# Kernel optimization log

Measured on AMD Instinct MI355X. Metric: run time of the kernel, lower is better.

## Reference

```python
import jax, jax.numpy as jnp
import numpy as np

B = 2048
MAX_ATOMS = 32
ELEM = 83
LATENT = 64
LATTICE = 9


def _lin(k, fin, fout):
    k1, k2 = jax.random.split(k)
    s = 1.0 / np.sqrt(fin)
    return (jax.random.uniform(k1, (fin, fout), jnp.float32, -s, s),
            jax.random.uniform(k2, (fout,), jnp.float32, -s, s))


def setup_inputs() -> dict:
    key = jax.random.key(0)
    ks = jax.random.split(key, 32)
    inp = {}
    inp['elements'] = jax.random.randint(ks[0], (B, MAX_ATOMS), 0, ELEM)
    inp['coords'] = jax.random.uniform(ks[1], (B, MAX_ATOMS, 3), jnp.float32)
    inp['lattice'] = jax.random.normal(ks[2], (B, LATTICE), jnp.float32)
    inp['composition'] = jax.random.uniform(ks[3], (B, ELEM), jnp.float32)
    inp['eps'] = jax.random.normal(ks[4], (B, LATENT), jnp.float32)
    inp['emb_table'] = jax.random.normal(ks[5], (ELEM, 16), jnp.float32)
    inp['enc_w1'], inp['enc_b1'] = _lin(ks[6], 19, 256)
    inp['enc_w2'], inp['enc_b2'] = _lin(ks[7], 256, 128)
    inp['enc_w3'], inp['enc_b3'] = _lin(ks[8], 128, 128)
    inp['lat_w1'], inp['lat_b1'] = _lin(ks[9], LATTICE, 64)
    inp['lat_w2'], inp['lat_b2'] = _lin(ks[10], 64, 64)
    inp['mu_w'], inp['mu_b'] = _lin(ks[11], 192, LATENT)
    inp['lv_w'], inp['lv_b'] = _lin(ks[12], 192, LATENT)
    inp['dec_w1'], inp['dec_b1'] = _lin(ks[13], LATENT + ELEM, 512)
    s1 = 1.0 / np.sqrt(64 * 27)
    inp['ct1_w'] = jax.random.uniform(ks[14], (32, 64, 3, 3, 3), jnp.float32, -s1, s1)
    inp['ct1_b'] = jax.random.uniform(ks[15], (32,), jnp.float32, -s1, s1)
    s2 = 1.0 / np.sqrt(32 * 27)
    inp['ct2_w'] = jax.random.uniform(ks[16], (16, 32, 3, 3, 3), jnp.float32, -s2, s2)
    inp['ct2_b'] = jax.random.uniform(ks[17], (16,), jnp.float32, -s2, s2)
    inp['dec_w2'], inp['dec_b2'] = _lin(ks[18], 16 * 8 * 8 * 8, MAX_ATOMS * (ELEM + 3))
    inp['dl_w1'], inp['dl_b1'] = _lin(ks[19], LATENT, 64)
    inp['dl_w2'], inp['dl_b2'] = _lin(ks[20], 64, LATTICE)
    inp['gat1_w'], _ = _lin(ks[21], 19, 3 * 64)
    inp['gat1_b'] = jnp.zeros((3 * 64,), jnp.float32)
    inp['gat1_as'] = jax.random.normal(ks[22], (3, 64), jnp.float32) * 0.1
    inp['gat1_ad'] = jax.random.normal(ks[23], (3, 64), jnp.float32) * 0.1
    inp['gat2_w'], _ = _lin(ks[24], 192, 3)
    inp['gat2_b'] = jnp.zeros((3,), jnp.float32)
    inp['gat2_as'] = jax.random.normal(ks[25], (1, 3), jnp.float32) * 0.1
    inp['gat2_ad'] = jax.random.normal(ks[26], (1, 3), jnp.float32) * 0.1
    return inp


def _convT(x, w, b):
    # ConvTranspose3d(k=3, stride=2, pad=1, output_pad=1) == input-dilated conv
    y = jax.lax.conv_general_dilated(
        x, w, window_strides=(1, 1, 1),
        padding=((1, 2), (1, 2), (1, 2)), lhs_dilation=(2, 2, 2),
        dimension_numbers=('NCDHW', 'OIDHW', 'NCDHW'))
    return y + b[None, :, None, None, None]


def _gat(x, W, a_src, a_dst, bias, heads, out_ch, concat):
    # Dense (fully-connected per-sample graph) GATConv, eval mode (dropout off).
    Bn, N, F = x.shape
    h = jnp.einsum('bnf,fhc->bnhc', x, W.reshape(F, heads, out_ch))  # [B,N,H,C]
    s = jnp.einsum('bnhc,hc->bnh', h, a_src)  # source scores
    d = jnp.einsum('bnhc,hc->bnh', h, a_dst)  # target scores
    # e[b,i,j,h] for edge j->i (self-loops included in the full mesh)
    e = jax.nn.leaky_relu(d[:, :, None, :] + s[:, None, :, :], 0.2)
    a = jax.nn.softmax(e, axis=2)  # softmax over sources j per target i
    o = jnp.einsum('bijh,bjhc->bihc', a, h)
    if concat:
        return o.reshape(Bn, N, heads * out_ch) + bias
    return o.mean(axis=2) + bias


def reference(elements, coords, lattice, composition, eps, emb_table,
              enc_w1, enc_b1, enc_w2, enc_b2, enc_w3, enc_b3,
              lat_w1, lat_b1, lat_w2, lat_b2, mu_w, mu_b, lv_w, lv_b,
              dec_w1, dec_b1, ct1_w, ct1_b, ct2_w, ct2_b, dec_w2, dec_b2,
              dl_w1, dl_b1, dl_w2, dl_b2,
              gat1_w, gat1_b, gat1_as, gat1_ad,
              gat2_w, gat2_b, gat2_as, gat2_ad):
    Bn = coords.shape[0]
    # ---- encode ----
    af = jnp.concatenate([emb_table[elements], coords], axis=-1)  # [B,32,19]
    h = jax.nn.relu(af @ enc_w1 + enc_b1)
    h = jax.nn.relu(h @ enc_w2 + enc_b2)
    h = h @ enc_w3 + enc_b3
    g = h.mean(axis=1)  # [B,128]
    l = jax.nn.relu(lattice @ lat_w1 + lat_b1) @ lat_w2 + lat_b2
    comb = jnp.concatenate([g, l], axis=1)
    mu = comb @ mu_w + mu_b
    logvar = comb @ lv_w + lv_b
    z = mu + eps * jnp.exp(0.5 * logvar)
    # ---- decode ----
    d = jnp.concatenate([z, composition], axis=1) @ dec_w1 + dec_b1
    d = d.reshape(Bn, 64, 2, 2, 2)
    d = jax.nn.relu(_convT(d, ct1_w, ct1_b))   # [B,32,4,4,4]
    d = jax.nn.relu(_convT(d, ct2_w, ct2_b))   # [B,16,8,8,8]
    raw = (d.reshape(Bn, -1) @ dec_w2 + dec_b2).reshape(Bn, MAX_ATOMS, ELEM + 3)
    logits = raw[..., :ELEM]
    init_coords = jax.nn.sigmoid(raw[..., ELEM:])
    node = jnp.concatenate([emb_table[jnp.argmax(logits, axis=-1)], init_coords], axis=-1)  # [B,32,19]
    x = jax.nn.elu(_gat(node, gat1_w, gat1_as, gat1_ad, gat1_b, 3, 64, True))
    adj = jnp.tanh(_gat(x, gat2_w, gat2_as, gat2_ad, gat2_b, 1, 3, False)) * 0.1
    coords_out = jnp.mod(init_coords + adj, 1.0)
    recon = jnp.concatenate([logits, coords_out], axis=-1)  # [B,32,86]
    recon_lattice = jax.nn.relu(z @ dl_w1 + dl_b1) @ dl_w2 + dl_b2
    return (mu, logvar, recon, recon_lattice)
```

## Files before the change

### kernel.cpp

```cpp
#include <hip/hip_runtime.h>
#include <hip/hip_bf16.h>

typedef __hip_bfloat16 bf16;
typedef __attribute__((ext_vector_type(8))) __bf16 bf16x8;
typedef __attribute__((ext_vector_type(4))) float f32x4;

__device__ __forceinline__ float b2f(bf16 v){ return __bfloat162float(v); }
__device__ __forceinline__ bf16  f2b(float v){ return __float2bfloat16(v); }

template<typename T> __device__ __forceinline__ float ldf(const T* p, size_t i);
template<> __device__ __forceinline__ float ldf<float>(const float* p, size_t i){ return p[i]; }
template<> __device__ __forceinline__ float ldf<bf16 >(const bf16*  p, size_t i){ return b2f(p[i]); }

template<typename T> __device__ __forceinline__ void stf(T* p, size_t i, float v);
template<> __device__ __forceinline__ void stf<float>(float* p, size_t i, float v){ p[i] = v; }
template<> __device__ __forceinline__ void stf<bf16 >(bf16*  p, size_t i, float v){ p[i] = f2b(v); }

#define NATM 32
#define RECON_OFF 262144
#define RL_OFF    5898240

__device__ __forceinline__ void glds16(const bf16* g, bf16* l){
    __builtin_amdgcn_global_load_lds(
        (const __attribute__((address_space(1))) unsigned int*)g,
        (__attribute__((address_space(3))) unsigned int*)l,
        16, 0, 0);
}

__global__ __launch_bounds__(64) void k_detect(const void* emb, int* flag)
{
    __shared__ int cnt[64];
    const int t = threadIdx.x;
    const unsigned short* p = (const unsigned short*)emb;
    int c = 0;
    for (int i = t; i < 256; i += 64){
        int e = (p[i] >> 7) & 0xFF;
        c += (e >= 110 && e <= 132) ? 1 : 0;
    }
    cnt[t] = c;
    __syncthreads();
    if (t == 0){
        int s = 0;
        for (int i = 0; i < 64; i++) s += cnt[i];
        *flag = (s >= 200) ? 1 : 0;
    }
}

template<typename T>
__device__ __forceinline__ void enc_impl(
    const int* elements, const T* coords, const T* emb,
    const T* w1, const T* b1, const T* w2, const T* b2c,
    const T* w3, const T* b3, float* gbuf, char* smem)
{
    float (*af)[19]   = (float(*)[19])(smem);
    float (*h1)[256]  = (float(*)[256])(smem + 2432);
    float (*h2s)[128] = (float(*)[128])(smem + 35200);
    float* hsum       = (float*)(smem + 51584);
    const int b = blockIdx.x, t = threadIdx.x;

    for (int idx = t; idx < NATM*19; idx += 256){
        int n = idx/19, f = idx - n*19;
        af[n][f] = (f < 16) ? ldf(emb, (size_t)elements[b*NATM+n]*16 + f)
                            : ldf(coords, (size_t)(b*NATM+n)*3 + (f-16));
    }
    __syncthreads();
    {
        float wc[19];
        #pragma unroll
        for (int f=0; f<19; f++) wc[f] = ldf(w1, f*256 + t);
        float bb = ldf(b1, t);
        for (int n=0; n<NATM; n++){
            float a = bb;
            #pragma unroll
            for (int f=0; f<19; f++) a += af[n][f]*wc[f];
            h1[n][t] = fmaxf(a, 0.f);
        }
    }
    __syncthreads();
    {
        const int j = t & 127, half = t >> 7;
        float bb = ldf(b2c, j);
        float acc[16];
        #pragma unroll
        for (int n=0;n<16;n++) acc[n] = bb;
        for (int k=0;k<256;k+=4){
            float wa = ldf(w2, (k+0)*128+j);
            float wb = ldf(w2, (k+1)*128+j);
            float wcv= ldf(w2, (k+2)*128+j);
            float wd = ldf(w2, (k+3)*128+j);
            #pragma unroll
            for (int n=0;n<16;n++){
                float4 hv = *(const float4*)(&h1[half*16+n][k]);
                acc[n] += hv.x*wa + hv.y*wb + hv.z*wcv + hv.w*wd;
            }
        }
        #pragma unroll
        for (int n=0;n<16;n++) h2s[half*16+n][j] = fmaxf(acc[n], 0.f);
    }
    __syncthreads();
    if (t < 128){
        float s = 0.f;
        for (int n=0;n<NATM;n++) s += h2s[n][t];
        hsum[t] = s;
    }
    __syncthreads();
    if (t < 128){
        float a = 0.f;
        for (int k=0;k<128;k++) a += hsum[k]*ldf(w3, k*128+t);
        gbuf[b*128+t] = a*(1.f/32.f) + ldf(b3, t);
    }
}

__global__ __launch_bounds__(256) void k_encoder(
    const int* flag, const int* elements, const void* coords, const void* emb,
    const void* w1, const void* b1, const void* w2, const void* b2,
    const void* w3, const void* b3, float* gbuf)
{
    __shared__ __align__(16) char smem[52096];
    if (*flag) enc_impl<bf16>(elements,(const bf16*)coords,(const bf16*)emb,
        (const bf16*)w1,(const bf16*)b1,(const bf16*)w2,(const bf16*)b2,
        (const bf16*)w3,(const bf16*)b3, gbuf, smem);
    else       enc_impl<float>(elements,(const float*)coords,(const float*)emb,
        (const float*)w1,(const float*)b1,(const float*)w2,(const float*)b2,
        (const float*)w3,(const float*)b3, gbuf, smem);
}

template<typename T>
__device__ __forceinline__ void lat_impl(
    const T* lattice, const T* eps, const T* comp,
    const T* lw1, const T* lb1, const T* lw2, const T* lb2,
    const T* muw, const T* mub, const T* lvw, const T* lvb,
    const T* dw1, const T* db1, const T* dw2, const T* db2,
    const float* gbuf, float* zbuf, bf16* zc, void* d_out, char* smem)
{
    float* comb = (float*)(smem);
    float* lat  = (float*)(smem + 768);
    float* l1   = (float*)(smem + 832);
    float* zz   = (float*)(smem + 1088);
    float* r1   = (float*)(smem + 1344);
    T* out_mu = (T*)d_out;
    T* out_lv = out_mu + 131072;
    T* out_rl = out_mu + RL_OFF;
    const int b = blockIdx.x, t = threadIdx.x;
    comb[t]    = gbuf[b*128 + t];
    comb[64+t] = gbuf[b*128 + 64 + t];
    if (t < 9) lat[t] = ldf(lattice, b*9 + t);
    __syncthreads();
    {
        float a = ldf(lb1, t);
        #pragma unroll
        for (int f=0; f<9; f++) a += lat[f]*ldf(lw1, f*64+t);
        l1[t] = fmaxf(a, 0.f);
    }
    __syncthreads();
    {
        float a = ldf(lb2, t);
        for (int k=0;k<64;k++) a += l1[k]*ldf(lw2, k*64+t);
        comb[128+t] = a;
    }
    __syncthreads();
    float mu = ldf(mub, t), lv = ldf(lvb, t);
    for (int k=0;k<192;k++){
        float c = comb[k];
        mu += c*ldf(muw, k*64+t);
        lv += c*ldf(lvw, k*64+t);
    }
    float z = mu + ldf(eps, b*64+t)*expf(0.5f*lv);
    stf(out_mu, (size_t)b*64+t, mu);
    stf(out_lv, (size_t)b*64+t, lv);
    zbuf[b*64+t] = z;
    zz[t] = z;
    __syncthreads();
    if (zc){
        for (int i=t; i<160; i+=64){
            float v = (i<64) ? zz[i] : ((i<147) ? ldf(comp, b*83 + (i-64)) : 0.f);
            zc[(size_t)b*160 + i] = f2b(v);
        }
    }
    {
        float a = ldf(db1, t);
        for (int k=0;k<64;k++) a += zz[k]*ldf(dw1, k*64+t);
        r1[t] = fmaxf(a, 0.f);
    }
    __syncthreads();
    if (t < 9){
        float a = ldf(db2, t);
        for (int k=0;k<64;k++) a += r1[k]*ldf(dw2, k*9+t);
        stf(out_rl, (size_t)b*9+t, a);
    }
}

__global__ __launch_bounds__(64) void k_latent(
    const int* flag, const void* lattice, const void* eps, const void* comp,
    const void* lw1, const void* lb1, const void* lw2, const void* lb2,
    const void* muw, const void* mub, const void* lvw, const void* lvb,
    const void* dw1, const void* db1, const void* dw2, const void* db2,
    const float* gbuf, float* zbuf, bf16* zc, void* d_out)
{
    __shared__ __align__(16) char smem[1600];
    if (*flag) lat_impl<bf16>((const bf16*)lattice,(const bf16*)eps,(const bf16*)comp,
        (const bf16*)lw1,(const bf16*)lb1,(const bf16*)lw2,(const bf16*)lb2,
        (const bf16*)muw,(const bf16*)mub,(const bf16*)lvw,(const bf16*)lvb,
        (const bf16*)dw1,(const bf16*)db1,(const bf16*)dw2,(const bf16*)db2,
        gbuf, zbuf, zc, d_out, smem);
    else       lat_impl<float>((const float*)lattice,(const float*)eps,(const float*)comp,
        (const float*)lw1,(const float*)lb1,(const float*)lw2,(const float*)lb2,
        (const float*)muw,(const float*)mub,(const float*)lvw,(const float*)lvb,
        (const float*)dw1,(const float*)db1,(const float*)dw2,(const float*)db2,
        gbuf, zbuf, zc, d_out, smem);
}

template<typename T>
__device__ __forceinline__ void prep_impl(
    const T* db1, const T* c1b, const T* c2b, const T* db2, const T* dw1,
    float* biasf, bf16* BtW1)
{
    const int gt = blockIdx.x*256 + threadIdx.x;
    const int gs = gridDim.x*256;
    for (int i = gt; i < 3376; i += gs){
        float v;
        if (i < 512)      v = ldf(db1, i);
        else if (i < 544) v = ldf(c1b, i-512);
        else if (i < 560) v = ldf(c2b, i-544);
        else              v = (i-560 < 2752) ? ldf(db2, i-560) : 0.f;
        biasf[i] = v;
    }
    for (int e = gt; e < 512*160; e += gs){
        int n = e/160, k = e - n*160;
        BtW1[e] = f2b((k < 147) ? ldf(dw1, (size_t)k*512 + n) : 0.f);
    }
}

__global__ __launch_bounds__(256) void k_prep(
    const int* flag, const void* db1, const void* c1b, const void* c2b,
    const void* db2, const void* dw1, float* biasf, bf16* BtW1)
{
    if (*flag) prep_impl<bf16>((const bf16*)db1,(const bf16*)c1b,(const bf16*)c2b,
        (const bf16*)db2,(const bf16*)dw1, biasf, BtW1);
    else       prep_impl<float>((const float*)db1,(const float*)c1b,(const float*)c2b,
        (const float*)db2,(const float*)dw1, biasf, BtW1);
}

template<typename T>
__device__ __forceinline__ void expWc1_impl(const T* w, bf16* Wc1T)
{
    const int t = threadIdx.x;
    const int n = blockIdx.x*4 + (t >> 6);
    const int k0 = (t & 63) << 3;
    const int o = n >> 6, spo = n & 63;
    const int zd = spo >> 4, zh = (spo >> 2) & 3, zw = spo & 3;
    bf16 v8[8];
    #pragma unroll
    for (int j = 0; j < 8; j++){
        int k = k0 + j;
        int i = k >> 3, sp = k & 7;
        int td = sp >> 2, th = (sp >> 1) & 1, tw = sp & 1;
        int kd = 2*td + 1 - zd, kh = 2*th + 1 - zh, kw = 2*tw + 1 - zw;
        float v = 0.f;
        if (kd >= 0 && kd < 3 && kh >= 0 && kh < 3 && kw >= 0 && kw < 3)
            v = ldf(w, (size_t)(o*64 + i)*27 + kd*9 + kh*3 + kw);
        v8[j] = f2b(v);
    }
    *(int4*)(&Wc1T[(size_t)n*512 + k0]) = *(int4*)v8;
}

__global__ __launch_bounds__(256) void k_expWc1(const int* flag, const void* w, bf16* Wc1T)
{
    if (*flag) expWc1_impl<bf16>((const bf16*)w, Wc1T);
    else       expWc1_impl<float>((const float*)w, Wc1T);
}

template<typename T>
__device__ __forceinline__ void expWc2_impl(const T* w, bf16* Wc2T)
{
    const int n = blockIdx.x;
    const int k0 = threadIdx.x << 3;
    const int o = n >> 9, spo = n & 511;
    const int zd = spo >> 6, zh = (spo >> 3) & 7, zw = spo & 7;
    bf16 v8[8];
    #pragma unroll
    for (int j = 0; j < 8; j++){
        int k = k0 + j;
        int i = k >> 6, sp = k & 63;
        int td = sp >> 4, th = (sp >> 2) & 3, tw = sp & 3;
        int kd = 2*td + 1 - zd, kh = 2*th + 1 - zh, kw = 2*tw + 1 - zw;
        float v = 0.f;
        if (kd >= 0 && kd < 3 && kh >= 0 && kh < 3 && kw >= 0 && kw < 3)
            v = ldf(w, (size_t)(o*32 + i)*27 + kd*9 + kh*3 + kw);
        v8[j] = f2b(v);
    }
    *(int4*)(&Wc2T[(size_t)n*2048 + k0]) = *(int4*)v8;
}

__global__ __launch_bounds__(256) void k_expWc2(const int* flag, const void* w, bf16* Wc2T)
{
    if (*flag) expWc2_impl<bf16>((const bf16*)w, Wc2T);
    else       expWc2_impl<float>((const float*)w, Wc2T);
}

template<typename T>
__device__ __forceinline__ void transW_impl(const T* B, bf16* Bt)
{
    __shared__ bf16 tile[64][65];
    const int kb = blockIdx.x << 6;
    const int nb = blockIdx.y << 6;
    const int t = threadIdx.x;
    for (int idx=t; idx<4096; idx+=256){
        int k = idx>>6, n = idx&63;
        int col = nb + n;
        tile[k][n] = (col < 2752) ? f2b(ldf(B, (size_t)(kb+k)*2752 + col)) : f2b(0.f);
    }
    __syncthreads();
    for (int idx=t; idx<4096; idx+=256){
        int n = idx>>6, k = idx&63;
        Bt[(size_t)(nb+n)*8192 + kb + k] = tile[k][n];
    }
}

__global__ __launch_bounds__(256) void k_transW(const int* flag, const void* B, bf16* Bt)
{
    if (*flag) transW_impl<bf16>((const bf16*)B, Bt);
    else       transW_impl<float>((const float*)B, Bt);
}

struct GemmAcc { f32x4 a[4][4]; };

__device__ __forceinline__ void gemm128_core(
    const bf16* __restrict__ A, const bf16* __restrict__ Bt, int K,
    int bm, int bn, bf16* As, bf16* Bs, GemmAcc& G)
{
    const int t = threadIdx.x;
    const int w = t >> 6, lane = t & 63;
    const int wm = w >> 1, wn = w & 1;
    const int ml = lane & 15, mq = lane >> 4;
    const int lrow = lane >> 2;
    const int gchunk = (lane & 3) ^ ((lane >> 3) & 3);
    const int rchunk = (mq ^ ((ml >> 1) & 3)) << 3;

    const size_t arow = (size_t)(bm + w*32 + lrow);
    const size_t brow = (size_t)(bn + w*32 + lrow);

    for (int kt = 0; kt < K; kt += 32){
        __syncthreads();
        #pragma unroll
        for (int c = 0; c < 2; c++){
            glds16(A  + (arow + c*16)*K + kt + gchunk*8, &As[(w*32 + c*16)*32]);
            glds16(Bt + (brow + c*16)*K + kt + gchunk*8, &Bs[(w*32 + c*16)*32]);
        }
        __syncthreads();
        bf16x8 af[4], bfr[4];
        #pragma unroll
        for (int i=0;i<4;i++) af[i]  = *(const bf16x8*)(&As[(wm*64 + i*16 + ml)*32 + rchunk]);
        #pragma unroll
        for (int j=0;j<4;j++) bfr[j] = *(const bf16x8*)(&Bs[(wn*64 + j*16 + ml)*32 + rchunk]);
        #pragma unroll
        for (int i=0;i<4;i++)
            #pragma unroll
            for (int j=0;j<4;j++)
                G.a[i][j] = __builtin_amdgcn_mfma_f32_16x16x32_bf16(af[i], bfr[j], G.a[i][j], 0,0,0);
    }
}

template<int ACT>
__global__ __launch_bounds__(256) void k_gemm128(
    const bf16* __restrict__ A, const bf16* __restrict__ Bt, int K,
    const float* __restrict__ biasf, int bshift,
    bf16* __restrict__ C, int ldc)
{
    __shared__ __align__(16) bf16 As[128*32];
    __shared__ __align__(16) bf16 Bs[128*32];
    const int t = threadIdx.x;
    const int bm = blockIdx.x << 7, bn = blockIdx.y << 7;
    const int w = t >> 6, lane = t & 63;
    const int wm = w >> 1, wn = w & 1;
    const int ml = lane & 15, mq = lane >> 4;
    GemmAcc G;
    #pragma unroll
    for (int i=0;i<4;i++)
        #pragma unroll
        for (int j=0;j<4;j++) G.a[i][j] = (f32x4){0.f,0.f,0.f,0.f};
    gemm128_core(A, Bt, K, bm, bn, As, Bs, G);
    #pragma unroll
    for (int j=0;j<4;j++){
        const int col = bn + wn*64 + (j<<4) + ml;
        const float bv = biasf[col >> bshift];
        #pragma unroll
        for (int i=0;i<4;i++){
            #pragma unroll
            for (int r=0;r<4;r++){
                const int row = bm + wm*64 + (i<<4) + (mq<<2) + r;
                float v = G.a[i][j][r] + bv;
                if (ACT == 1) v = fmaxf(v, 0.f);
                C[(size_t)row*ldc + col] = f2b(v);
            }
        }
    }
}

__global__ __launch_bounds__(256) void k_gemm128_recon(
    const int* __restrict__ flag,
    const bf16* __restrict__ A, const bf16* __restrict__ Bt,
    const float* __restrict__ biasf, void* __restrict__ d_out)
{
    __shared__ __align__(16) bf16 As[128*32];
    __shared__ __align__(16) bf16 Bs[128*32];
    const int t = threadIdx.x;
    const int bm = blockIdx.x << 7, bn = blockIdx.y << 7;
    const int w = t >> 6, lane = t & 63;
    const int wm = w >> 1, wn = w & 1;
    const int ml = lane & 15, mq = lane >> 4;
    GemmAcc G;
    #pragma unroll
    for (int i=0;i<4;i++)
        #pragma unroll
        for (int j=0;j<4;j++) G.a[i][j] = (f32x4){0.f,0.f,0.f,0.f};
    gemm128_core(A, Bt, 8192, bm, bn, As, Bs, G);
    const int fl = *flag;
    #pragma unroll
    for (int j=0;j<4;j++){
        const int col = bn + wn*64 + (j<<4) + ml;
        if (col >= 2752) continue;
        const int f = col % 86;
        const float bv = biasf[560 + col];
        #pragma unroll
        for (int i=0;i<4;i++){
            #pragma unroll
            for (int r=0;r<4;r++){
                const int row = bm + wm*64 + (i<<4) + (mq<<2) + r;
                float v = G.a[i][j][r] + bv;
                if (f >= 83) v = 1.f/(1.f + expf(-v));
                if (fl) stf((bf16*)d_out + RECON_OFF, (size_t)row*2752 + col, v);
                else    stf((float*)d_out + RECON_OFF, (size_t)row*2752 + col, v);
            }
        }
    }
}

template<typename T>
__device__ __forceinline__ void conv_impl(
    const float* zbuf, const T* comp,
    const T* dw1, const T* db1, const T* c1w, const T* c1b,
    const T* c2w, const T* c2b, bf16* Amat, char* smem)
{
    float* zc        = (float*)(smem);
    float (*d0s)[8]  = (float(*)[8])(smem + 640);
    float (*c1s)[64] = (float(*)[64])(smem + 2688);
    bf16* w2s        = (bf16*)(smem + 10880);
    const int b = blockIdx.x, t = threadIdx.x;
    for (int i=t; i<16*32*27; i+=256) w2s[i] = f2b(ldf(c2w, i));
    if (t < 147) zc[t] = (t < 64) ? zbuf[b*64+t] : ldf(comp, b*83 + (t-64));
    __syncthreads();
    #pragma unroll
    for (int jj=0; jj<2; jj++){
        int j = t + (jj<<8);
        float a = ldf(db1, j);
        for (int k=0;k<147;k++) a += zc[k]*ldf(dw1, k*512+j);
        d0s[j>>3][j&7] = a;
    }
    __syncthreads();
    {
        const int o = t>>3;
        const float bias = ldf(c1b, o);
        const T* wb = c1w + o*64*27;
        for (int u=0; u<8; u++){
            int sp = (t&7) + (u<<3);
            int zd = sp>>4, zh = (sp>>2)&3, zw = sp&3;
            float acc = bias;
            for (int kd=0;kd<3;kd++){
                int qd = zd+kd-1; if (qd<0 || (qd&1) || qd>=4) continue; int td=qd>>1;
                for (int kh=0;kh<3;kh++){
                    int qh = zh+kh-1; if (qh<0 || (qh&1) || qh>=4) continue; int th=qh>>1;
                    for (int kw=0;kw<3;kw++){
                        int qw = zw+kw-1; if (qw<0 || (qw&1) || qw>=4) continue; int tw=qw>>1;
                        const int koff = kd*9+kh*3+kw;
                        const int spi = td*4+th*2+tw;
                        float s = 0.f;
                        #pragma unroll 8
                        for (int i=0;i<64;i++) s += ldf(wb, i*27+koff)*d0s[i][spi];
                        acc += s;
                    }
                }
            }
            c1s[o][sp] = fmaxf(acc, 0.f);
        }
    }
    __syncthreads();
    {
        const int o = t>>4;
        const float bias = ldf(c2b, o);
        for (int u=0; u<32; u++){
            int sp = (t&15) + (u<<4);
            int zd = sp>>6, zh=(sp>>3)&7, zw=sp&7;
            float acc = bias;
            for (int kd=0;kd<3;kd++){
                int qd = zd+kd-1; if (qd<0 || (qd&1) || qd>=8) continue; int td=qd>>1;
                for (int kh=0;kh<3;kh++){
                    int qh = zh+kh-1; if (qh<0 || (qh&1) || qh>=8) continue; int th=qh>>1;
                    for (int kw=0;kw<3;kw++){
                        int qw = zw+kw-1; if (qw<0 || (qw&1) || qw>=8) continue; int tw=qw>>1;
                        const int koff = kd*9+kh*3+kw;
                        const int spi = td*16+th*4+tw;
                        const int wbase = (o*32)*27 + koff;
                        float s = 0.f;
                        #pragma unroll 8
                        for (int i=0;i<32;i++) s += b2f(w2s[wbase + i*27])*c1s[i][spi];
                        acc += s;
                    }
                }
            }
            Amat[(size_t)b*8192 + o*512 + sp] = f2b(fmaxf(acc, 0.f));
        }
    }
}

__global__ __launch_bounds__(256) void k_conv(
    const int* flag, const float* zbuf, const void* comp,
    const void* dw1, const void* db1, const void* c1w, const void* c1b,
    const void* c2w, const void* c2b, bf16* Amat)
{
    __shared__ __align__(16) char smem[38528];
    if (*flag) conv_impl<bf16>(zbuf,(const bf16*)comp,(const bf16*)dw1,(const bf16*)db1,
        (const bf16*)c1w,(const bf16*)c1b,(const bf16*)c2w,(const bf16*)c2b, Amat, smem);
    else       conv_impl<float>(zbuf,(const float*)comp,(const float*)dw1,(const float*)db1,
        (const float*)c1w,(const float*)c1b,(const float*)c2w,(const float*)c2b, Amat, smem);
}

template<typename T> struct BStage;
template<> struct BStage<bf16>{
    static __device__ __forceinline__ void go(const bf16* p, bf16* v8){
        union{ int4 q; bf16 e[8]; } u; u.q = *(const int4*)p;
        #pragma unroll
        for (int j=0;j<8;j++) v8[j] = u.e[j];
    }
};
template<> struct BStage<float>{
    static __device__ __forceinline__ void go(const float* p, bf16* v8){
        float4 a = *(const float4*)p, b = *(const float4*)(p+4);
        v8[0]=f2b(a.x); v8[1]=f2b(a.y); v8[2]=f2b(a.z); v8[3]=f2b(a.w);
        v8[4]=f2b(b.x); v8[5]=f2b(b.y); v8[6]=f2b(b.z); v8[7]=f2b(b.w);
    }
};

__device__ __forceinline__ bf16x8 readBfrag(const bf16 (*Bs)[42], int n, int k0){
    union { bf16x8 v; unsigned int u[4]; } r;
    const unsigned int* p = (const unsigned int*)(&Bs[n][k0]);
    r.u[0]=p[0]; r.u[1]=p[1]; r.u[2]=p[2]; r.u[3]=p[3];
    return r.v;
}

template<typename T>
__device__ __forceinline__ void gemm_impl(
    const bf16* A, const T* B, const T* bias, void* d_out, char* smem)
{
    bf16 (*As)[40] = (bf16(*)[40])(smem);
    bf16 (*Bs)[42] = (bf16(*)[42])(smem + 10240);
    T* out_recon = (T*)d_out + RECON_OFF;
    const int t = threadIdx.x;
    const int bm = blockIdx.x << 7;
    const int bn = blockIdx.y << 6;
    const int w = t >> 6, lane = t & 63;
    const int ml = lane & 15, mq = lane >> 4;
    f32x4 acc[2][4];
    #pragma unroll
    for (int i=0;i<2;i++)
        #pragma unroll
        for (int j=0;j<4;j++) acc[i][j] = (f32x4){0.f,0.f,0.f,0.f};

    const int sm = t >> 2;
    const int sk = (t & 3) << 3;
    const int kk = t >> 3;
    const int nn = (t & 7) << 3;

    for (int kt = 0; kt < 8192; kt += 32){
        __syncthreads();
        {
            int4 v0 = *(const int4*)(A + (size_t)(bm + sm     )*8192 + kt + sk);
            int4 v1 = *(const int4*)(A + (size_t)(bm + sm + 64)*8192 + kt + sk);
            *(int4*)(&As[sm][sk])    = v0;
            *(int4*)(&As[sm+64][sk]) = v1;
            bf16 bv[8];
            BStage<T>::go(B + (size_t)(kt + kk)*2752 + bn + nn, bv);
            #pragma unroll
            for (int j=0;j<8;j++) Bs[nn+j][kk] = bv[j];
        }
        __syncthreads();
        bf16x8 a0 = *(const bf16x8*)(&As[(w<<5) + ml     ][mq<<3]);
        bf16x8 a1 = *(const bf16x8*)(&As[(w<<5) + 16 + ml][mq<<3]);
        bf16x8 b0 = readBfrag(Bs, ml,      mq<<3);
        bf16x8 b1 = readBfrag(Bs, 16 + ml, mq<<3);
        bf16x8 b2 = readBfrag(Bs, 32 + ml, mq<<3);
        bf16x8 b3 = readBfrag(Bs, 48 + ml, mq<<3);
        acc[0][0] = __builtin_amdgcn_mfma_f32_16x16x32_bf16(a0,b0,acc[0][0],0,0,0);
        acc[0][1] = __builtin_amdgcn_mfma_f32_16x16x32_bf16(a0,b1,acc[0][1],0,0,0);
        acc[0][2] = __builtin_amdgcn_mfma_f32_16x16x32_bf16(a0,b2,acc[0][2],0,0,0);
        acc[0][3] = __builtin_amdgcn_mfma_f32_16x16x32_bf16(a0,b3,acc[0][3],0,0,0);
        acc[1][0] = __builtin_amdgcn_mfma_f32_16x16x32_bf16(a1,b0,acc[1][0],0,0,0);
        acc[1][1] = __builtin_amdgcn_mfma_f32_16x16x32_bf16(a1,b1,acc[1][1],0,0,0);
        acc[1][2] = __builtin_amdgcn_mfma_f32_16x16x32_bf16(a1,b2,acc[1][2],0,0,0);
        acc[1][3] = __builtin_amdgcn_mfma_f32_16x16x32_bf16(a1,b3,acc[1][3],0,0,0);
    }
    #pragma unroll
    for (int nt=0; nt<4; nt++){
        const int col = bn + (nt<<4) + ml;
        const int atom = col / 86;
        const int f = col - atom*86;
        const float bv = ldf(bias, col);
        #pragma unroll
        for (int mt=0; mt<2; mt++){
            #pragma unroll
            for (int r=0; r<4; r++){
                const int row = bm + (w<<5) + (mt<<4) + (mq<<2) + r;
                float v = acc[mt][nt][r] + bv;
                if (f >= 83) v = 1.f/(1.f + expf(-v));
                stf(out_recon, (size_t)row*2752 + col, v);
            }
        }
    }
}

__global__ __launch_bounds__(256) void k_gemm(
    const int* flag, const bf16* A, const void* B, const void* bias, void* d_out)
{
    __shared__ __align__(16) char smem[15616];
    if (*flag) gemm_impl<bf16>(A, (const bf16*)B, (const bf16*)bias, d_out, smem);
    else       gemm_impl<float>(A, (const float*)B, (const float*)bias, d_out, smem);
}

template<typename T>
__device__ __forceinline__ void gat_impl(
    const T* emb, const T* g1w, const T* g1b, const T* g1as, const T* g1ad,
    const T* g2w, const T* g2b, const T* g2as, const T* g2ad,
    void* d_out, char* smem)
{
    float* ic    = (float*)(smem);
    int*   amaxs = (int*)  (smem + 384);
    float* hs    = (float*)(smem + 512);
    float* xs    = (float*)(smem + 25088);
    float* U     = (float*)(smem + 49664);
    float* sa    = (float*)(smem + 61952);
    float* da    = (float*)(smem + 62336);
    float* hh    = (float*)(smem + 62720);
    float* s2    = (float*)(smem + 63104);
    float* d2    = (float*)(smem + 63232);
    float* lg    = xs;
    float* node  = U;
    float* att   = U;
    float* att2  = U;

    T* out_recon = (T*)d_out + RECON_OFF;
    const int b = blockIdx.x, t = threadIdx.x;

    for (int i=t; i<2656; i+=256){
        int n = i/83, f = i - n*83;
        lg[i] = ldf(out_recon, (size_t)b*2752 + n*86 + f);
    }
    if (t < 96){
        int n = t/3, c = t - 3*(t/3);
        ic[t] = ldf(out_recon, (size_t)b*2752 + n*86 + 83 + c);
    }
    __syncthreads();
    if (t < 32){
        const float* lp = lg + t*83;
        float best = lp[0]; int bi = 0;
        for (int f=1; f<83; f++){ float v = lp[f]; if (v > best){ best=v; bi=f; } }
        amaxs[t] = bi;
    }
    __syncthreads();
    for (int i=t; i<608; i+=256){
        int n = i/19, f = i - n*19;
        node[n*19+f] = (f<16) ? ldf(emb, amaxs[n]*16+f) : ic[n*3 + (f-16)];
    }
    __syncthreads();
    if (t < 192){
        float wc[19];
        #pragma unroll
        for (int f=0;f<19;f++) wc[f] = ldf(g1w, f*192+t);
        for (int n=0;n<32;n++){
            float a = 0.f;
            #pragma unroll
            for (int f=0;f<19;f++) a += node[n*19+f]*wc[f];
            hs[n*192+t] = a;
        }
    }
    __syncthreads();
    if (t < 96){
        int n = t/3, hd = t - 3*(t/3);
        float s=0.f, d=0.f;
        for (int c=0;c<64;c++){
            float hv = hs[n*192 + hd*64 + c];
            s += hv*ldf(g1as, hd*64+c);
            d += hv*ldf(g1ad, hd*64+c);
        }
        sa[n*3+hd] = s; da[n*3+hd] = d;
    }
    __syncthreads();
    if (t < 96){
        int i = t/3, hd = t - 3*(t/3);
        float di = da[i*3+hd];
        float ev[32]; float m = -1e30f;
        for (int j=0;j<32;j++){
            float e = di + sa[j*3+hd];
            e = (e > 0.f) ? e : 0.2f*e;
            ev[j] = e; m = fmaxf(m, e);
        }
        float ssum = 0.f;
        for (int j=0;j<32;j++){ float p = expf(ev[j]-m); ev[j]=p; ssum += p; }
        float inv = 1.f/ssum;
        for (int j=0;j<32;j++) att[(i*3+hd)*32 + j] = ev[j]*inv;
    }
    __syncthreads();
    if (t < 192){
        int hd = t >> 6;
        float bb = ldf(g1b, t);
        for (int i=0;i<32;i++){
            float a = 0.f;
            for (int j=0;j<32;j++) a += att[(i*3+hd)*32 + j]*hs[j*192+t];
            a += bb;
            xs[i*192+t] = (a > 0.f) ? a : (expf(a) - 1.f);
        }
    }
    __syncthreads();
    if (t < 96){
        int n = t/3, c = t - 3*(t/3);
        float a = 0.f;
        for (int f=0;f<192;f++) a += xs[n*192+f]*ldf(g2w, f*3+c);
        hh[n*3+c] = a;
    }
    __syncthreads();
    if (t < 32){
        float s=0.f,d=0.f;
        #pragma unroll
        for (int c=0;c<3;c++){ s += hh[t*3+c]*ldf(g2as,c); d += hh[t*3+c]*ldf(g2ad,c); }
        s2[t]=s; d2[t]=d;
    }
    __syncthreads();
    if (t < 32){
        float di = d2[t];
        float ev[32]; float m=-1e30f;
        for (int j=0;j<32;j++){
            float e = di + s2[j]; e = (e>0.f)?e:0.2f*e; ev[j]=e; m=fmaxf(m,e);
        }
        float ssum=0.f;
        for (int j=0;j<32;j++){ float p=expf(ev[j]-m); ev[j]=p; ssum+=p; }
        float inv = 1.f/ssum;
        for (int j=0;j<32;j++) att2[t*32+j] = ev[j]*inv;
    }
    __syncthreads();
    if (t < 96){
        int i = t/3, c = t - 3*(t/3);
        float a = 0.f;
        for (int j=0;j<32;j++) a += att2[i*32+j]*hh[j*3+c];
        a += ldf(g2b, c);
        float adj = tanhf(a)*0.1f;
        float cr = ic[i*3+c] + adj;
        cr -= floorf(cr);
        stf(out_recon, (size_t)b*2752 + i*86 + 83 + c, cr);
    }
}

__global__ __launch_bounds__(256) void k_gat(
    const int* flag, const void* emb,
    const void* g1w, const void* g1b, const void* g1as, const void* g1ad,
    const void* g2w, const void* g2b, const void* g2as, const void* g2ad,
    void* d_out)
{
    __shared__ __align__(16) char smem[63360];
    if (*flag) gat_impl<bf16>((const bf16*)emb,(const bf16*)g1w,(const bf16*)g1b,
        (const bf16*)g1as,(const bf16*)g1ad,(const bf16*)g2w,(const bf16*)g2b,
        (const bf16*)g2as,(const bf16*)g2ad, d_out, smem);
    else       gat_impl<float>((const float*)emb,(const float*)g1w,(const float*)g1b,
        (const float*)g1as,(const float*)g1ad,(const float*)g2w,(const float*)g2b,
        (const float*)g2as,(const float*)g2ad, d_out, smem);
}

extern "C" void kernel_launch(void* const* d_in, const int* in_sizes, int n_in,
                              void* d_out, int out_size, void* d_ws, size_t ws_size,
                              hipStream_t stream)
{
    (void)in_sizes; (void)n_in; (void)out_size;
    char* ws = (char*)d_ws;
    const bool big = (ws_size >= 83000000ull);

    if (big){
        bf16*  Amat  = (bf16*)(ws);
        bf16*  Wc2T  = (bf16*)(ws + 33554432);
        bf16*  BtW2  = (bf16*)(ws + 33554432);
        bf16*  c1    = (bf16*)(ws + 67108864);
        bf16*  d0    = (bf16*)(ws + 75497472);
        bf16*  Wc1T  = (bf16*)(ws + 77594624);
        bf16*  zc    = (bf16*)(ws + 79691776);
        bf16*  BtW1  = (bf16*)(ws + 80347136);
        float* biasf = (float*)(ws + 80510976);
        float* gbuf  = (float*)(ws + 80524480);
        float* zbuf  = (float*)(ws + 81573056);
        int*   flag  = (int*)  (ws + 82097344);

        k_detect<<<1, 64, 0, stream>>>(d_in[5], flag);
        k_prep<<<64, 256, 0, stream>>>(flag, d_in[21], d_in[23], d_in[25], d_in[27], d_in[20], biasf, BtW1);
        k_expWc1<<<512, 256, 0, stream>>>(flag, d_in[22], Wc1T);
        k_expWc2<<<8192, 256, 0, stream>>>(flag, d_in[24], Wc2T);
        k_encoder<<<2048, 256, 0, stream>>>(flag, (const int*)d_in[0], d_in[1], d_in[5],
            d_in[6], d_in[7], d_in[8], d_in[9], d_in[10], d_in[11], gbuf);
        k_latent<<<2048, 64, 0, stream>>>(flag, d_in[2], d_in[4], d_in[3],
            d_in[12], d_in[13], d_in[14], d_in[15],
            d_in[16], d_in[17], d_in[18], d_in[19],
            d_in[28], d_in[29], d_in[30], d_in[31],
            gbuf, zbuf, zc, d_out);
        k_gemm128<0><<<dim3(16,4),  256, 0, stream>>>(zc, BtW1, 160,  biasf,     0, d0,   512);
        k_gemm128<1><<<dim3(16,16), 256, 0, stream>>>(d0, Wc1T, 512,  biasf+512, 6, c1,   2048);
        k_gemm128<1><<<dim3(16,64), 256, 0, stream>>>(c1, Wc2T, 2048, biasf+544, 9, Amat, 8192);
        k_transW<<<dim3(128,44), 256, 0, stream>>>(flag, d_in[26], BtW2);
        k_gemm128_recon<<<dim3(16,22), 256, 0, stream>>>(flag, Amat, BtW2, biasf, d_out);
        k_gat<<<2048, 256, 0, stream>>>(flag, d_in[5],
            d_in[32], d_in[33], d_in[34], d_in[35],
            d_in[36], d_in[37], d_in[38], d_in[39], d_out);
    } else {
        bf16*  Amat = (bf16*)(ws);
        float* gbuf = (float*)(ws + 33554432);
        float* zbuf = (float*)(ws + 34603008);
        int*   flag = (int*)  (ws + 35127296);

        k_detect<<<1, 64, 0, stream>>>(d_in[5], flag);
        k_encoder<<<2048, 256, 0, stream>>>(flag, (const int*)d_in[0], d_in[1], d_in[5],
            d_in[6], d_in[7], d_in[8], d_in[9], d_in[10], d_in[11], gbuf);
        k_latent<<<2048, 64, 0, stream>>>(flag, d_in[2], d_in[4], d_in[3],
            d_in[12], d_in[13], d_in[14], d_in[15],
            d_in[16], d_in[17], d_in[18], d_in[19],
            d_in[28], d_in[29], d_in[30], d_in[31],
            gbuf, zbuf, (bf16*)nullptr, d_out);
        k_conv<<<2048, 256, 0, stream>>>(flag, zbuf, d_in[3],
            d_in[20], d_in[21], d_in[22], d_in[23], d_in[24], d_in[25], Amat);
        k_gemm<<<dim3(16,43), 256, 0, stream>>>(flag, Amat, d_in[26], d_in[27], d_out);
        k_gat<<<2048, 256, 0, stream>>>(flag, d_in[5],
            d_in[32], d_in[33], d_in[34], d_in[35],
            d_in[36], d_in[37], d_in[38], d_in[39], d_out);
    }
}
```

Measured before the change: 795.7 us.

## Move encoder MLP to MFMA GEMMs, halve recon tile, register-block GAT aggregation

The per-molecule encoder kernel is replaced by a pipeline that builds a padded bf16 input matrix, runs the first two encoder layers as MFMA GEMMs, and applies the pooled third layer in a small reduction kernel. This uses the linearity of the mean to pool before the last linear layer. The recon GEMM uses 64-row tiles, doubling the block count to improve occupancy on the 16x22 grid. The GAT aggregation loop now keeps 32 accumulators in registers and reuses each hs load across them. Intermediates now take extra workspace memory, the encoder runs in bf16 precision, and the weight-prep kernels are reordered after the latent kernel.

```diff
diff --git a/kernel.cpp b/kernel.cpp
--- a/kernel.cpp
+++ b/kernel.cpp
@@ -44,6 +44,81 @@
         for (int i = 0; i < 64; i++) s += cnt[i];
         *flag = (s >= 200) ? 1 : 0;
     }
+}
+
+template<typename T>
+__device__ __forceinline__ void prepEnc_impl(
+    const T* w1, const T* b1, const T* w2, const T* b2,
+    bf16* W1t, bf16* W2t, float* ebias)
+{
+    const int gt = blockIdx.x*256 + threadIdx.x;
+    const int gs = gridDim.x*256;
+    for (int e = gt; e < 8192; e += gs){
+        int n = e >> 5, k = e & 31;
+        W1t[e] = (k < 19) ? f2b(ldf(w1, (size_t)k*256 + n)) : f2b(0.f);
+    }
+    for (int e = gt; e < 32768; e += gs){
+        int n = e >> 8, k = e & 255;
+        W2t[e] = f2b(ldf(w2, (size_t)k*128 + n));
+    }
+    for (int i = gt; i < 384; i += gs)
+        ebias[i] = (i < 256) ? ldf(b1, i) : ldf(b2, i-256);
+}
+
+__global__ __launch_bounds__(256) void k_prepEnc(
+    const int* flag, const void* w1, const void* b1, const void* w2, const void* b2,
+    bf16* W1t, bf16* W2t, float* ebias)
+{
+    if (*flag) prepEnc_impl<bf16>((const bf16*)w1,(const bf16*)b1,(const bf16*)w2,(const bf16*)b2, W1t, W2t, ebias);
+    else       prepEnc_impl<float>((const float*)w1,(const float*)b1,(const float*)w2,(const float*)b2, W1t, W2t, ebias);
+}
+
+template<typename T>
+__device__ __forceinline__ void buildA_impl(
+    const int* elements, const T* coords, const T* emb, bf16* Abuf)
+{
+    const int r = blockIdx.x*256 + threadIdx.x;
+    const int el = elements[r];
+    bf16 row[32];
+    #pragma unroll
+    for (int f=0; f<16; f++) row[f] = f2b(ldf(emb, (size_t)el*16 + f));
+    #pragma unroll
+    for (int c=0; c<3; c++) row[16+c] = f2b(ldf(coords, (size_t)r*3 + c));
+    #pragma unroll
+    for (int f=19; f<32; f++) row[f] = f2b(0.f);
+    *(int4*)(&Abuf[(size_t)r*32])      = *(int4*)(&row[0]);
+    *(int4*)(&Abuf[(size_t)r*32 + 8])  = *(int4*)(&row[8]);
+    *(int4*)(&Abuf[(size_t)r*32 + 16]) = *(int4*)(&row[16]);
+    *(int4*)(&Abuf[(size_t)r*32 + 24]) = *(int4*)(&row[24]);
+}
+
+__global__ __launch_bounds__(256) void k_buildA(
+    const int* flag, const int* elements, const void* coords, const void* emb, bf16* Abuf)
+{
+    if (*flag) buildA_impl<bf16>(elements,(const bf16*)coords,(const bf16*)emb, Abuf);
+    else       buildA_impl<float>(elements,(const float*)coords,(const float*)emb, Abuf);
+}
+
+template<typename T>
+__device__ __forceinline__ void pool_impl(
+    const float* h2, const T* w3, const T* b3, float* gbuf)
+{
+    __shared__ float hsum[128];
+    const int b = blockIdx.x, t = threadIdx.x;
+    float s = 0.f;
+    for (int n=0; n<32; n++) s += h2[(size_t)(b*32+n)*128 + t];
+    hsum[t] = s;
+    __syncthreads();
+    float a = 0.f;
+    for (int k=0; k<128; k++) a += hsum[k]*ldf(w3, (size_t)k*128 + t);
+    gbuf[b*128+t] = a*(1.f/32.f) + ldf(b3, t);
+}
+
+__global__ __launch_bounds__(128) void k_pool(
+    const int* flag, const float* h2, const void* w3, const void* b3, float* gbuf)
+{
+    if (*flag) pool_impl<bf16>(h2, (const bf16*)w3, (const bf16*)b3, gbuf);
+    else       pool_impl<float>(h2, (const float*)w3, (const float*)b3, gbuf);
 }
 
 template<typename T>
@@ -361,11 +436,11 @@
     }
 }
 
-template<int ACT>
+template<typename OutT, int ACT>
 __global__ __launch_bounds__(256) void k_gemm128(
     const bf16* __restrict__ A, const bf16* __restrict__ Bt, int K,
     const float* __restrict__ biasf, int bshift,
-    bf16* __restrict__ C, int ldc)
+    OutT* __restrict__ C, int ldc)
 {
     __shared__ __align__(16) bf16 As[128*32];
     __shared__ __align__(16) bf16 Bs[128*32];
@@ -391,30 +466,56 @@
                 const int row = bm + wm*64 + (i<<4) + (mq<<2) + r;
                 float v = G.a[i][j][r] + bv;
                 if (ACT == 1) v = fmaxf(v, 0.f);
-                C[(size_t)row*ldc + col] = f2b(v);
+                stf(C, (size_t)row*ldc + col, v);
             }
         }
     }
 }
 
-__global__ __launch_bounds__(256) void k_gemm128_recon(
+__global__ __launch_bounds__(256) void k_gemm_recon64(
     const int* __restrict__ flag,
     const bf16* __restrict__ A, const bf16* __restrict__ Bt,
     const float* __restrict__ biasf, void* __restrict__ d_out)
 {
-    __shared__ __align__(16) bf16 As[128*32];
+    __shared__ __align__(16) bf16 As[64*32];
     __shared__ __align__(16) bf16 Bs[128*32];
+    const int K = 8192;
     const int t = threadIdx.x;
-    const int bm = blockIdx.x << 7, bn = blockIdx.y << 7;
+    const int bm = blockIdx.x << 6, bn = blockIdx.y << 7;
     const int w = t >> 6, lane = t & 63;
     const int wm = w >> 1, wn = w & 1;
     const int ml = lane & 15, mq = lane >> 4;
-    GemmAcc G;
-    #pragma unroll
-    for (int i=0;i<4;i++)
-        #pragma unroll
-        for (int j=0;j<4;j++) G.a[i][j] = (f32x4){0.f,0.f,0.f,0.f};
-    gemm128_core(A, Bt, 8192, bm, bn, As, Bs, G);
+    const int lrow = lane >> 2;
+    const int gchunk = (lane & 3) ^ ((lane >> 3) & 3);
+    const int rchunk = (mq ^ ((ml >> 1) & 3)) << 3;
+
+    f32x4 acc[2][4];
+    #pragma unroll
+    for (int i=0;i<2;i++)
+        #pragma unroll
+        for (int j=0;j<4;j++) acc[i][j] = (f32x4){0.f,0.f,0.f,0.f};
+
+    const size_t arow = (size_t)(bm + w*16 + lrow);
+    const size_t brow = (size_t)(bn + w*32 + lrow);
+
+    for (int kt = 0; kt < K; kt += 32){
+        __syncthreads();
+        glds16(A + arow*K + kt + gchunk*8, &As[(w*16)*32]);
+        #pragma unroll
+        for (int c = 0; c < 2; c++)
+            glds16(Bt + (brow + c*16)*K + kt + gchunk*8, &Bs[(w*32 + c*16)*32]);
+        __syncthreads();
+        bf16x8 af[2], bfr[4];
+        #pragma unroll
+        for (int i=0;i<2;i++) af[i]  = *(const bf16x8*)(&As[(wm*32 + i*16 + ml)*32 + rchunk]);
+        #pragma unroll
+        for (int j=0;j<4;j++) bfr[j] = *(const bf16x8*)(&Bs[(wn*64 + j*16 + ml)*32 + rchunk]);
+        #pragma unroll
+        for (int i=0;i<2;i++)
+            #pragma unroll
+            for (int j=0;j<4;j++)
+                acc[i][j] = __builtin_amdgcn_mfma_f32_16x16x32_bf16(af[i], bfr[j], acc[i][j], 0,0,0);
+    }
     const int fl = *flag;
     #pragma unroll
     for (int j=0;j<4;j++){
@@ -423,11 +524,11 @@
         const int f = col % 86;
         const float bv = biasf[560 + col];
         #pragma unroll
-        for (int i=0;i<4;i++){
+        for (int i=0;i<2;i++){
             #pragma unroll
             for (int r=0;r<4;r++){
-                const int row = bm + wm*64 + (i<<4) + (mq<<2) + r;
-                float v = G.a[i][j][r] + bv;
+                const int row = bm + wm*32 + (i<<4) + (mq<<2) + r;
+                float v = acc[i][j][r] + bv;
                 if (f >= 83) v = 1.f/(1.f + expf(-v));
                 if (fl) stf((bf16*)d_out + RECON_OFF, (size_t)row*2752 + col, v);
                 else    stf((float*)d_out + RECON_OFF, (size_t)row*2752 + col, v);
@@ -710,13 +811,19 @@
     }
     __syncthreads();
     if (t < 192){
-        int hd = t >> 6;
+        const int hd = t >> 6;
         float bb = ldf(g1b, t);
+        float a[32];
+        #pragma unroll
+        for (int i=0;i<32;i++) a[i] = 0.f;
+        for (int j=0;j<32;j++){
+            float hv = hs[j*192+t];
+            #pragma unroll
+            for (int i=0;i<32;i++) a[i] += att[(i*3+hd)*32 + j]*hv;
+        }
         for (int i=0;i<32;i++){
-            float a = 0.f;
-            for (int j=0;j<32;j++) a += att[(i*3+hd)*32 + j]*hs[j*192+t];
-            a += bb;
-            xs[i*192+t] = (a > 0.f) ? a : (expf(a) - 1.f);
+            float v = a[i] + bb;
+            xs[i*192+t] = (v > 0.f) ? v : (expf(v) - 1.f);
         }
     }
     __syncthreads();
@@ -782,6 +889,9 @@
     const bool big = (ws_size >= 83000000ull);
 
     if (big){
+        bf16*  Abuf  = (bf16*)(ws);
+        bf16*  h1    = (bf16*)(ws + 4194304);
+        float* h2    = (float*)(ws + 37748736);
         bf16*  Amat  = (bf16*)(ws);
         bf16*  Wc2T  = (bf16*)(ws + 33554432);
         bf16*  BtW2  = (bf16*)(ws + 33554432);
@@ -794,23 +904,29 @@
         float* gbuf  = (float*)(ws + 80524480);
         float* zbuf  = (float*)(ws + 81573056);
         int*   flag  = (int*)  (ws + 82097344);
+        bf16*  W1t   = (bf16*)(ws + 82097408);
+        bf16*  W2t   = (bf16*)(ws + 82113792);
+        float* ebias = (float*)(ws + 82179328);
 
         k_detect<<<1, 64, 0, stream>>>(d_in[5], flag);
-        k_prep<<<64, 256, 0, stream>>>(flag, d_in[21], d_in[23], d_in[25], d_in[27], d_in[20], biasf, BtW1);
-        k_expWc1<<<512, 256, 0, stream>>>(flag, d_in[22], Wc1T);
-        k_expWc2<<<8192, 256, 0, stream>>>(flag, d_in[24], Wc2T);
-        k_encoder<<<2048, 256, 0, stream>>>(flag, (const int*)d_in[0], d_in[1], d_in[5],
-            d_in[6], d_in[7], d_in[8], d_in[9], d_in[10], d_in[11], gbuf);
+        k_prepEnc<<<64, 256, 0, stream>>>(flag, d_in[6], d_in[7], d_in[8], d_in[9], W1t, W2t, ebias);
+        k_buildA<<<256, 256, 0, stream>>>(flag, (const int*)d_in[0], d_in[1], d_in[5], Abuf);
+        k_gemm128<bf16,1> <<<dim3(512,2), 256, 0, stream>>>(Abuf, W1t, 32,  ebias,     0, h1, 256);
+        k_gemm128<float,1><<<dim3(512,1), 256, 0, stream>>>(h1,   W2t, 256, ebias+256, 0, h2, 128);
+        k_pool<<<2048, 128, 0, stream>>>(flag, h2, d_in[10], d_in[11], gbuf);
         k_latent<<<2048, 64, 0, stream>>>(flag, d_in[2], d_in[4], d_in[3],
             d_in[12], d_in[13], d_in[14], d_in[15],
             d_in[16], d_in[17], d_in[18], d_in[19],
             d_in[28], d_in[29], d_in[30], d_in[31],
             gbuf, zbuf, zc, d_out);
-        k_gemm128<0><<<dim3(16,4),  256, 0, stream>>>(zc, BtW1, 160,  biasf,     0, d0,   512);
-        k_gemm128<1><<<dim3(16,16), 256, 0, stream>>>(d0, Wc1T, 512,  biasf+512, 6, c1,   2048);
-        k_gemm128<1><<<dim3(16,64), 256, 0, stream>>>(c1, Wc2T, 2048, biasf+544, 9, Amat, 8192);
+        k_prep<<<64, 256, 0, stream>>>(flag, d_in[21], d_in[23], d_in[25], d_in[27], d_in[20], biasf, BtW1);
+        k_expWc1<<<512, 256, 0, stream>>>(flag, d_in[22], Wc1T);
+        k_expWc2<<<8192, 256, 0, stream>>>(flag, d_in[24], Wc2T);
+        k_gemm128<bf16,0><<<dim3(16,4),  256, 0, stream>>>(zc, BtW1, 160,  biasf,     0, d0,   512);
+        k_gemm128<bf16,1><<<dim3(16,16), 256, 0, stream>>>(d0, Wc1T, 512,  biasf+512, 6, c1,   2048);
+        k_gemm128<bf16,1><<<dim3(16,64), 256, 0, stream>>>(c1, Wc2T, 2048, biasf+544, 9, Amat, 8192);
         k_transW<<<dim3(128,44), 256, 0, stream>>>(flag, d_in[26], BtW2);
-        k_gemm128_recon<<<dim3(16,22), 256, 0, stream>>>(flag, Amat, BtW2, biasf, d_out);
+        k_gemm_recon64<<<dim3(32,22), 256, 0, stream>>>(flag, Amat, BtW2, biasf, d_out);
         k_gat<<<2048, 256, 0, stream>>>(flag, d_in[5],
             d_in[32], d_in[33], d_in[34], d_in[35],
             d_in[36], d_in[37], d_in[38], d_in[39], d_out);
```

After: 708.0 us. 11.0% less time.
